# Optimization experiments

Measured on AMD Instinct MI355X. Metric: run time of the kernel, lower is better.

The kernel has to match this reference:

```python
import jax, jax.numpy as jnp
import numpy as np


def _make_grid(h, w, stride=1):
    """Vectorized port of gen_grid_coordinates_exp. Returns (1, 3*Ho, 3*Wo, 2) float32,
    last dim = (x_norm, y_norm) in [-1,1] (torch grid_sample convention)."""
    rows = np.arange(0, h, stride)
    cols = np.arange(0, w, stride)
    theta = -((rows + 0.5) / h * np.pi - np.pi / 2)          # (Ho,)
    phi = (cols + 0.5) / w * 2 * np.pi - np.pi               # (Wo,)
    dtheta = np.pi / h
    dphi = 2 * np.pi / w
    # 3x3 tangent-plane offsets (du: horizontal, dv: vertical), per get_exp_duv
    du = np.tan(dphi) * np.array([[-1., 0., 1.]] * 3)                      # (3,3)
    dv = np.tan(dtheta) * np.array([[1., 1., 1.], [0., 0., 0.], [-1., -1., -1.]])
    T = theta[:, None, None, None]   # (Ho,1,1,1)
    P = phi[None, :, None, None]     # (1,Wo,1,1)
    u_x = -du * np.sin(P) - dv * np.sin(T) * np.cos(P)       # (Ho,Wo,3,3)
    u_y = du * np.cos(P) - dv * np.sin(T) * np.sin(P)
    u_z = dv * np.cos(T) + np.zeros_like(u_x)
    u_norm = np.sqrt(u_x ** 2 + u_y ** 2 + u_z ** 2)
    u_div = np.where(u_norm == 0, 1.0, u_norm)
    c, s = np.cos(u_norm), np.sin(u_norm)
    ex = np.cos(T) * np.cos(P) * c + u_x / u_div * s
    ey = np.cos(T) * np.sin(P) * c + u_y / u_div * s
    ez = np.sin(T) * c + u_z / u_div * s
    new_phi = np.arctan2(ey, ex)
    new_theta = np.arcsin(np.clip(ez, -1.0, 1.0))
    new_r = (-new_theta + np.pi / 2) * h / np.pi - 0.5
    new_c = ((new_phi + np.pi) * w / (2 * np.pi) - 0.5 + w) % w
    # kernel center samples the original integer pixel exactly
    new_r[:, :, 1, 1] = rows[:, None]
    new_c[:, :, 1, 1] = cols[None, :]
    gx = new_c * 2.0 / w - 1.0
    gy = new_r * 2.0 / h - 1.0
    grid = np.stack([gx, gy], axis=-1)                        # (Ho,Wo,3,3,2)
    Ho, Wo = len(rows), len(cols)
    grid = grid.transpose(0, 2, 1, 3, 4).reshape(1, Ho * 3, Wo * 3, 2)
    return grid.astype(np.float32)


def _grid_sample_bilinear(x, grid):
    """torch.nn.functional.grid_sample(mode='bilinear', padding='zeros', align_corners=False).
    x: (B,C,H,W); grid: (1,Hg,Wg,2) shared across batch."""
    B, C, H, W = x.shape
    gx = grid[0, ..., 0]
    gy = grid[0, ..., 1]
    Hg, Wg = gx.shape
    ix = ((gx + 1.0) * W - 1.0) * 0.5   # unnormalize, align_corners=False
    iy = ((gy + 1.0) * H - 1.0) * 0.5
    x0 = jnp.floor(ix); x1 = x0 + 1.0
    y0 = jnp.floor(iy); y1 = y0 + 1.0
    xf = x.reshape(B, C, H * W)

    def corner(xc, yc, wgt):
        valid = (xc >= 0) & (xc < W) & (yc >= 0) & (yc < H)
        xi = jnp.clip(xc, 0, W - 1).astype(jnp.int32)
        yi = jnp.clip(yc, 0, H - 1).astype(jnp.int32)
        idx = (yi * W + xi).reshape(-1)                      # (Hg*Wg,)
        w_eff = (wgt * valid.astype(wgt.dtype)).reshape(-1)  # zero-pad OOB
        return xf[:, :, idx] * w_eff                          # (B,C,Hg*Wg)

    out = (corner(x0, y0, (x1 - ix) * (y1 - iy))
           + corner(x1, y0, (ix - x0) * (y1 - iy))
           + corner(x0, y1, (x1 - ix) * (iy - y0))
           + corner(x1, y1, (ix - x0) * (iy - y0)))
    return out.reshape(B, C, Hg, Wg)


def setup_inputs() -> dict:
    key = jax.random.key(0)
    k1, k2 = jax.random.split(key)
    B, Cin, Cout, H, W = 4, 128, 256, 128, 256
    x = jax.random.normal(k1, (B, Cin, H, W), dtype=jnp.float32)
    # kaiming_uniform_(a=sqrt(5)) -> U(-1/sqrt(fan_in), 1/sqrt(fan_in)), fan_in = Cin*9
    bound = 1.0 / np.sqrt(Cin * 9)
    weight = jax.random.uniform(k2, (Cout, Cin, 3, 3), dtype=jnp.float32,
                                minval=-bound, maxval=bound)
    bias = jnp.zeros((Cout,), dtype=jnp.float32)
    grid = jnp.asarray(_make_grid(H, W, stride=1))  # (1, 3H, 3W, 2)
    return {"x": x, "weight": weight, "bias": bias, "grid": grid}


def reference(x, weight, bias, grid):
    sampled = _grid_sample_bilinear(x, grid)                 # (B,C,3H,3W)
    out = jax.lax.conv_general_dilated(
        sampled, weight, window_strides=(3, 3), padding='VALID',
        dimension_numbers=('NCHW', 'OIHW', 'NCHW'))          # (B,Cout,H,W)
    return out + bias[None, :, None, None]
```

## Files before the change

kernel.cpp:

```cpp
#include <hip/hip_runtime.h>


#define Hh   128
#define Ww   256
#define HWp  (Hh*Ww)
#define CIN  128
#define COUT 256
#define KTOT 1152
#define NPTS (384*768)
#define BM   128
#define BN   256
#define BK   32
#define NKS  (KTOT/BK)

typedef __attribute__((ext_vector_type(8))) __bf16 bf16x8;
typedef __attribute__((ext_vector_type(4))) float  f32x4;

__global__ void build_table(const float* __restrict__ grid,
                            int2* __restrict__ tI, float4* __restrict__ tW) {
    int g = blockIdx.x * 256 + threadIdx.x;
    if (g >= NPTS) return;
    int hh = g / 768, ww = g - hh * 768;
    int ho = hh / 3, ii = hh - 3 * ho;
    int wo = ww / 3, jj = ww - 3 * wo;

    float gx = grid[2 * g + 0];
    float gy = grid[2 * g + 1];
    float ix = ((gx + 1.0f) * (float)Ww - 1.0f) * 0.5f;
    float iy = ((gy + 1.0f) * (float)Hh - 1.0f) * 0.5f;
    float x0f = floorf(ix), y0f = floorf(iy);
    int x0 = (int)x0f, y0 = (int)y0f;
    float wx1 = ix - x0f, wx0 = 1.0f - wx1;
    float wy1 = iy - y0f, wy0 = 1.0f - wy1;

    float wyt = (y0 >= 0 && y0 < Hh) ? wy0 : 0.0f;
    float wyb = (y0 + 1 >= 0 && y0 + 1 < Hh) ? wy1 : 0.0f;
    int r0 = min(max(y0, 0), Hh - 1);
    int r1 = min(max(y0 + 1, 0), Hh - 1);

    int xb; float cw0, cw1;
    if (x0 < 0)            { xb = 0;      cw0 = wx1; cw1 = 0.0f; }
    else if (x0 > Ww - 2)  { xb = Ww - 2; cw0 = 0.0f; cw1 = wx0; }
    else                   { xb = x0;     cw0 = wx0; cw1 = wx1; }

    int e = (ho * Ww + wo) * 9 + ii * 3 + jj;
    tI[e] = make_int2(r0 * Ww + xb, r1 * Ww + xb);
    tW[e] = make_float4(cw0 * wyt, cw1 * wyt, cw0 * wyb, cw1 * wyb);
}

__global__ void conv_w(const float* __restrict__ w, __bf16* __restrict__ wt) {
    int o = blockIdx.x * 256 + threadIdx.x;
    if (o >= NKS * COUT * BK) return;
    int kk = o & (BK - 1);
    int n  = (o >> 5) & (COUT - 1);
    int ks = o >> 13;
    wt[o] = (__bf16)w[n * KTOT + ks * BK + kk];
}

__global__ __launch_bounds__(512, 2) void sphconv_gemm(
    const float* __restrict__ x, const __bf16* __restrict__ wt,
    const float* __restrict__ bias, const int2* __restrict__ tI,
    const float4* __restrict__ tW, float* __restrict__ out) {

    __shared__ int2   sTI[BM * 9];
    __shared__ float4 sTW[BM * 9];
    __shared__ __align__(16) __bf16 sA[BM * 40];
    __shared__ __align__(16) __bf16 sB[BN * 40];

    const int t   = threadIdx.x;
    const int m0  = blockIdx.x * BM;
    const int b   = m0 >> 15;
    const int sp0 = m0 & (HWp - 1);
    const float* xb_ = x + (size_t)b * (CIN * HWp);

    for (int e = t; e < BM * 9; e += 512) {
        sTI[e] = tI[sp0 * 9 + e];
        sTW[e] = tW[sp0 * 9 + e];
    }

    const int lane = t & 63;
    const int wid  = t >> 6;
    const int wrow = wid >> 2;
    const int wcol = wid & 3;
    const int quad = lane >> 4;
    const int l16  = lane & 15;

    const int mr_s = t & 127;
    const int kg   = t >> 7;

    f32x4 acc[4][4];
#pragma unroll
    for (int r = 0; r < 4; ++r)
#pragma unroll
        for (int c = 0; c < 4; ++c) {
            f32x4 z = {0.0f, 0.0f, 0.0f, 0.0f};
            acc[r][c] = z;
        }

    __syncthreads();

    for (int ks = 0; ks < NKS; ++ks) {
        int k  = ks * BK + kg * 8;
        int ci = k / 9;
        int ij = k - ci * 9;
        const float* img = xb_ + ci * HWp;
        bf16x8 av;
#pragma unroll
        for (int j = 0; j < 8; ++j) {
            int2   o  = sTI[mr_s * 9 + ij];
            float4 wv = sTW[mr_s * 9 + ij];
            float a0 = img[o.x], a1 = img[o.x + 1];
            float b0 = img[o.y], b1 = img[o.y + 1];
            float v = a0 * wv.x + a1 * wv.y + b0 * wv.z + b1 * wv.w;
            av[j] = (__bf16)v;
            if (++ij == 9) { ij = 0; img += HWp; }
        }
        *(bf16x8*)(&sA[mr_s * 40 + kg * 8]) = av;

        {
            const __bf16* src = wt + ks * (COUT * BK) + t * 16;
            bf16x8 v0 = *(const bf16x8*)(src);
            bf16x8 v1 = *(const bf16x8*)(src + 8);
            int n  = t >> 1;
            int kq = (t & 1) * 16;
            *(bf16x8*)(&sB[n * 40 + kq])     = v0;
            *(bf16x8*)(&sB[n * 40 + kq + 8]) = v1;
        }
        __syncthreads();

        bf16x8 af[4], bfr[4];
#pragma unroll
        for (int r = 0; r < 4; ++r)
            af[r] = *(const bf16x8*)(&sA[(wrow * 64 + r * 16 + l16) * 40 + quad * 8]);
#pragma unroll
        for (int c = 0; c < 4; ++c)
            bfr[c] = *(const bf16x8*)(&sB[(wcol * 64 + c * 16 + l16) * 40 + quad * 8]);
#pragma unroll
        for (int r = 0; r < 4; ++r)
#pragma unroll
            for (int c = 0; c < 4; ++c)
                acc[r][c] = __builtin_amdgcn_mfma_f32_16x16x32_bf16(
                    af[r], bfr[c], acc[r][c], 0, 0, 0);
        __syncthreads();
    }

#pragma unroll
    for (int c = 0; c < 4; ++c) {
        int n = wcol * 64 + c * 16 + l16;
        float bv = bias[n];
        float* outn = out + (((size_t)(b * COUT + n)) << 15) + sp0;
#pragma unroll
        for (int r = 0; r < 4; ++r) {
            int mbase = wrow * 64 + r * 16 + quad * 4;
#pragma unroll
            for (int i = 0; i < 4; ++i)
                outn[mbase + i] = acc[r][c][i] + bv;
        }
    }
}

extern "C" void kernel_launch(void* const* d_in, const int* in_sizes, int n_in,
                              void* d_out, int out_size, void* d_ws, size_t ws_size,
                              hipStream_t stream) {
    const float* x    = (const float*)d_in[0];
    const float* w    = (const float*)d_in[1];
    const float* bias = (const float*)d_in[2];
    const float* grid = (const float*)d_in[3];
    float* out = (float*)d_out;

    char* ws = (char*)d_ws;
    int2*   tI = (int2*)(ws);
    float4* tW = (float4*)(ws + 2359296);
    __bf16* wt = (__bf16*)(ws + 7077888);

    build_table<<<(NPTS + 255) / 256, 256, 0, stream>>>(grid, tI, tW);
    conv_w<<<(NKS * COUT * BK + 255) / 256, 256, 0, stream>>>(w, wt);
    sphconv_gemm<<<(4 * HWp) / BM, 512, 0, stream>>>(x, wt, bias, tI, tW, out);
}
```

Before: 415.9 us.

## Reorder GEMM K dimension tap-major and read sampling table from registers

Result: slower. 662.9 us (+59.4%).

```diff
diff --git a/kernel.cpp b/kernel.cpp
--- a/kernel.cpp
+++ b/kernel.cpp
@@ -43,7 +43,7 @@
     else if (x0 > Ww - 2)  { xb = Ww - 2; cw0 = 0.0f; cw1 = wx0; }
     else                   { xb = x0;     cw0 = wx0; cw1 = wx1; }
 
-    int e = (ho * Ww + wo) * 9 + ii * 3 + jj;
+    int e = (ii * 3 + jj) * HWp + (ho * Ww + wo);
     tI[e] = make_int2(r0 * Ww + xb, r1 * Ww + xb);
     tW[e] = make_float4(cw0 * wyt, cw1 * wyt, cw0 * wyb, cw1 * wyb);
 }
@@ -54,16 +54,16 @@
     int kk = o & (BK - 1);
     int n  = (o >> 5) & (COUT - 1);
     int ks = o >> 13;
-    wt[o] = (__bf16)w[n * KTOT + ks * BK + kk];
+    int ci = ((ks & 3) << 5) + kk;
+    int ij = ks >> 2;
+    wt[o] = (__bf16)w[n * KTOT + ci * 9 + ij];
 }
 
-__global__ __launch_bounds__(512, 2) void sphconv_gemm(
+__global__ __launch_bounds__(512, 4) void sphconv_gemm(
     const float* __restrict__ x, const __bf16* __restrict__ wt,
     const float* __restrict__ bias, const int2* __restrict__ tI,
     const float4* __restrict__ tW, float* __restrict__ out) {
 
-    __shared__ int2   sTI[BM * 9];
-    __shared__ float4 sTW[BM * 9];
     __shared__ __align__(16) __bf16 sA[BM * 40];
     __shared__ __align__(16) __bf16 sB[BN * 40];
 
@@ -72,11 +72,6 @@
     const int b   = m0 >> 15;
     const int sp0 = m0 & (HWp - 1);
     const float* xb_ = x + (size_t)b * (CIN * HWp);
-
-    for (int e = t; e < BM * 9; e += 512) {
-        sTI[e] = tI[sp0 * 9 + e];
-        sTW[e] = tW[sp0 * 9 + e];
-    }
 
     const int lane = t & 63;
     const int wid  = t >> 6;
@@ -87,6 +82,10 @@
 
     const int mr_s = t & 127;
     const int kg   = t >> 7;
+    const int sp   = sp0 + mr_s;
+
+    const int nB   = t >> 1;
+    const int kqB  = (t & 1) * 16;
 
     f32x4 acc[4][4];
 #pragma unroll
@@ -97,51 +96,49 @@
             acc[r][c] = z;
         }
 
-    __syncthreads();
+    for (int ij = 0; ij < 9; ++ij) {
+        const int2   o  = tI[ij * HWp + sp];
+        const float4 wv = tW[ij * HWp + sp];
 
-    for (int ks = 0; ks < NKS; ++ks) {
-        int k  = ks * BK + kg * 8;
-        int ci = k / 9;
-        int ij = k - ci * 9;
-        const float* img = xb_ + ci * HWp;
-        bf16x8 av;
+        for (int s = 0; s < 4; ++s) {
+            const int ks = ij * 4 + s;
+
+            const __bf16* srcB = wt + ks * (COUT * BK) + t * 16;
+            bf16x8 v0 = *(const bf16x8*)(srcB);
+            bf16x8 v1 = *(const bf16x8*)(srcB + 8);
+
+            const float* img = xb_ + (size_t)((s << 5) + (kg << 3)) * HWp;
+            bf16x8 av;
 #pragma unroll
-        for (int j = 0; j < 8; ++j) {
-            int2   o  = sTI[mr_s * 9 + ij];
-            float4 wv = sTW[mr_s * 9 + ij];
-            float a0 = img[o.x], a1 = img[o.x + 1];
-            float b0 = img[o.y], b1 = img[o.y + 1];
-            float v = a0 * wv.x + a1 * wv.y + b0 * wv.z + b1 * wv.w;
-            av[j] = (__bf16)v;
-            if (++ij == 9) { ij = 0; img += HWp; }
-        }
-        *(bf16x8*)(&sA[mr_s * 40 + kg * 8]) = av;
+            for (int j = 0; j < 8; ++j) {
+                float2 p0, p1;
+                __builtin_memcpy(&p0, img + o.x, 8);
+                __builtin_memcpy(&p1, img + o.y, 8);
+                av[j] = (__bf16)(p0.x * wv.x + p0.y * wv.y +
+                                 p1.x * wv.z + p1.y * wv.w);
+                img += HWp;
+            }
 
-        {
-            const __bf16* src = wt + ks * (COUT * BK) + t * 16;
-            bf16x8 v0 = *(const bf16x8*)(src);
-            bf16x8 v1 = *(const bf16x8*)(src + 8);
-            int n  = t >> 1;
-            int kq = (t & 1) * 16;
-            *(bf16x8*)(&sB[n * 40 + kq])     = v0;
-            *(bf16x8*)(&sB[n * 40 + kq + 8]) = v1;
-        }
-        __syncthreads();
+            *(bf16x8*)(&sA[mr_s * 40 + kg * 8]) = av;
+            *(bf16x8*)(&sB[nB * 40 + kqB])      = v0;
+            *(bf16x8*)(&sB[nB * 40 + kqB + 8])  = v1;
+            __syncthreads();
 
-        bf16x8 af[4], bfr[4];
+            bf16x8 af[4], bfr[4];
 #pragma unroll
-        for (int r = 0; r < 4; ++r)
-            af[r] = *(const bf16x8*)(&sA[(wrow * 64 + r * 16 + l16) * 40 + quad * 8]);
-#pragma unroll
-        for (int c = 0; c < 4; ++c)
-            bfr[c] = *(const bf16x8*)(&sB[(wcol * 64 + c * 16 + l16) * 40 + quad * 8]);
-#pragma unroll
-        for (int r = 0; r < 4; ++r)
+            for (int r = 0; r < 4; ++r)
+                af[r] = *(const bf16x8*)(&sA[(wrow * 64 + r * 16 + l16) * 40 + quad * 8]);
 #pragma unroll
             for (int c = 0; c < 4; ++c)
-                acc[r][c] = __builtin_amdgcn_mfma_f32_16x16x32_bf16(
-                    af[r], bfr[c], acc[r][c], 0, 0, 0);
-        __syncthreads();
+                bfr[c] = *(const bf16x8*)(&sB[(wcol * 64 + c * 16 + l16) * 40 + quad * 8]);
+#pragma unroll
+            for (int r = 0; r < 4; ++r)
+#pragma unroll
+                for (int c = 0; c < 4; ++c)
+                    acc[r][c] = __builtin_amdgcn_mfma_f32_16x16x32_bf16(
+                        af[r], bfr[c], acc[r][c], 0, 0, 0);
+            __syncthreads();
+        }
     }
 
 #pragma unroll
```
